# Optimization experiments

Hardware: AMD Instinct MI355X
Metric: run time of the kernel (lower is better)

The kernel has to match this reference:

```python
import jax, jax.numpy as jnp
import numpy as np

N_NODES = 100000
N_EDGES = 1600000
HIDDEN = 128


def setup_inputs() -> dict:
    key = jax.random.key(0)
    ks = jax.random.split(key, 10)
    inp = {
        "hidden_states": jax.random.normal(ks[0], (N_NODES, HIDDEN), dtype=jnp.float32),
        "edges_i": jax.random.randint(ks[1], (2, N_EDGES), 0, N_NODES, dtype=jnp.int64),
        "edges_ii": jax.random.randint(ks[2], (2, N_EDGES), 0, N_NODES, dtype=jnp.int64),
        "edges_iii": jax.random.randint(ks[3], (2, N_EDGES), 0, N_NODES, dtype=jnp.int64),
        "edges_a": jax.random.randint(ks[4], (2, N_EDGES), 0, N_NODES, dtype=jnp.int64),
        # GCNConv weights (hidden -> hidden), no bias, Glorot-like init
        "W_i": jax.random.normal(ks[5], (HIDDEN, HIDDEN), dtype=jnp.float32) / np.sqrt(HIDDEN),
        "W_ii": jax.random.normal(ks[6], (HIDDEN, HIDDEN), dtype=jnp.float32) / np.sqrt(HIDDEN),
        "W_iii": jax.random.normal(ks[7], (HIDDEN, HIDDEN), dtype=jnp.float32) / np.sqrt(HIDDEN),
        "W_a": jax.random.normal(ks[8], (HIDDEN, HIDDEN), dtype=jnp.float32) / np.sqrt(HIDDEN),
    }
    return inp


def _gcn_conv(x, W, edges):
    # GCNConv with normalize=False, add_self_loops=False, bias=False:
    # out[dst] = sum over edges (x @ W)[src]
    xw = x @ W                                   # [N, H] small GEMM
    msg = jnp.take(xw, edges[0], axis=0)         # gather at src: [E, H]
    return jax.ops.segment_sum(msg, edges[1], num_segments=x.shape[0])


def reference(hidden_states, edges_i, edges_ii, edges_iii, edges_a, W_i, W_ii, W_iii, W_a):
    # VariationalNormalEpanechnikovDropout acts as identity in eval mode.
    x = hidden_states
    out = _gcn_conv(x, W_i, edges_i)
    out = out + _gcn_conv(x, W_ii, edges_ii)
    out = out + _gcn_conv(x, W_iii, edges_iii)
    out = out + _gcn_conv(x, W_a, edges_a)
    return out
```

## Files before the change

### kernel.cpp

```cpp
#include <hip/hip_runtime.h>


#define H 128

typedef __bf16 bf16x8 __attribute__((ext_vector_type(8)));
typedef float f32x4 __attribute__((ext_vector_type(4)));

static __device__ __forceinline__ ushort f2bf(float f) {
  union { float f; uint u; } v; v.f = f;
  uint r = (v.u + 0x7FFFu + ((v.u >> 16) & 1u)) >> 16;
  return (ushort)r;
}
static __device__ __forceinline__ float bflo(uint u) {
  union { uint u; float f; } v; v.u = u << 16; return v.f;
}
static __device__ __forceinline__ float bfhi(uint u) {
  union { uint u; float f; } v; v.u = u & 0xFFFF0000u; return v.f;
}

__global__ __launch_bounds__(256) void prep_w(const float* __restrict__ W0,
                                              const float* __restrict__ W1,
                                              const float* __restrict__ W2,
                                              const float* __restrict__ W3,
                                              ushort* __restrict__ Wt) {
  int idx = blockIdx.x * 256 + threadIdx.x;
  int kk = idx & 127;
  int c = (idx >> 7) & 127;
  int k = idx >> 14;
  const float* W = (k == 0) ? W0 : (k == 1) ? W1 : (k == 2) ? W2 : W3;
  Wt[idx] = f2bf(W[kk * 128 + c]);
}

__global__ __launch_bounds__(256) void conv_x(const float4* __restrict__ X4,
                                              uint2* __restrict__ Xb2, int m) {
  int i = blockIdx.x * 256 + threadIdx.x;
  if (i < m) {
    float4 v = X4[i];
    uint2 p;
    p.x = (uint)f2bf(v.x) | ((uint)f2bf(v.y) << 16);
    p.y = (uint)f2bf(v.z) | ((uint)f2bf(v.w) << 16);
    Xb2[i] = p;
  }
}

static __device__ __forceinline__ void fetch_edge(
    int gid, int c1, int c2, int c3,
    const int* d0, const int* d1, const int* d2, const int* d3,
    const int* s0, const int* s1, const int* s2, const int* s3,
    int& dst, int& src, int& k) {
  int i;
  const int *dp, *sp;
  if (gid < c1)      { k = 0; i = gid;      dp = d0; sp = s0; }
  else if (gid < c2) { k = 1; i = gid - c1; dp = d1; sp = s1; }
  else if (gid < c3) { k = 2; i = gid - c2; dp = d2; sp = s2; }
  else               { k = 3; i = gid - c3; dp = d3; sp = s3; }
  dst = dp[i];
  src = sp[i];
}

#define EPB 4096

__global__ __launch_bounds__(256) void part_count(
    const int* __restrict__ d0, const int* __restrict__ d1,
    const int* __restrict__ d2, const int* __restrict__ d3,
    int c1, int c2, int c3, int tot, int nbin, int* __restrict__ hb) {
  __shared__ int lh[512];
  for (int i = threadIdx.x; i < nbin; i += 256) lh[i] = 0;
  __syncthreads();
  int base = blockIdx.x * EPB;
#pragma unroll
  for (int u = 0; u < 16; ++u) {
    int gid = base + u * 256 + threadIdx.x;
    if (gid < tot) {
      int i;
      const int* dp;
      if (gid < c1)      { i = gid;      dp = d0; }
      else if (gid < c2) { i = gid - c1; dp = d1; }
      else if (gid < c3) { i = gid - c2; dp = d2; }
      else               { i = gid - c3; dp = d3; }
      atomicAdd(&lh[dp[i] >> 8], 1);
    }
  }
  __syncthreads();
  int* row = hb + (size_t)blockIdx.x * nbin;
  for (int i = threadIdx.x; i < nbin; i += 256) row[i] = lh[i];
}

__global__ __launch_bounds__(256) void part_scanA(int* __restrict__ hb,
                                                  int nblk, int nbin,
                                                  int* __restrict__ btot) {
  __shared__ int ws4[4];
  const int bin = blockIdx.x;
  const int t = threadIdx.x, lane = t & 63, wid = t >> 6;
  const int C = (nblk + 255) / 256;
  int b0 = t * C;
  int b1 = min(b0 + C, nblk);
  int s = 0;
  for (int b = b0; b < b1; ++b) s += hb[(size_t)b * nbin + bin];
  int incl = s;
#pragma unroll
  for (int d = 1; d < 64; d <<= 1) {
    int x = __shfl_up(incl, d, 64);
    if (lane >= d) incl += x;
  }
  if (lane == 63) ws4[wid] = incl;
  __syncthreads();
  if (t == 0) {
    int run = 0;
#pragma unroll
    for (int i = 0; i < 4; ++i) { int v = ws4[i]; ws4[i] = run; run += v; }
  }
  __syncthreads();
  int run = ws4[wid] + (incl - s);
  for (int b = b0; b < b1; ++b) {
    int v = hb[(size_t)b * nbin + bin];
    hb[(size_t)b * nbin + bin] = run;
    run += v;
  }
  if (t == 255) btot[bin] = run;
}

__global__ __launch_bounds__(512) void part_scanB(const int* __restrict__ btot,
                                                  int* __restrict__ binbase,
                                                  int nbin) {
  __shared__ int ws8[8];
  const int t = threadIdx.x, lane = t & 63, wid = t >> 6;
  int v = (t < nbin) ? btot[t] : 0;
  int incl = v;
#pragma unroll
  for (int d = 1; d < 64; d <<= 1) {
    int x = __shfl_up(incl, d, 64);
    if (lane >= d) incl += x;
  }
  if (lane == 63) ws8[wid] = incl;
  __syncthreads();
  if (t == 0) {
    int run = 0;
#pragma unroll
    for (int i = 0; i < 8; ++i) { int v2 = ws8[i]; ws8[i] = run; run += v2; }
  }
  __syncthreads();
  int excl = ws8[wid] + (incl - v);
  if (t < nbin) binbase[t] = excl;
  if (t == nbin - 1) binbase[nbin] = excl + v;
}

__global__ __launch_bounds__(256) void part_scatter(
    const int* __restrict__ d0, const int* __restrict__ d1,
    const int* __restrict__ d2, const int* __restrict__ d3,
    const int* __restrict__ s0, const int* __restrict__ s1,
    const int* __restrict__ s2, const int* __restrict__ s3,
    int c1, int c2, int c3, int tot, int nbin,
    const int* __restrict__ hb, const int* __restrict__ binbase,
    uint* __restrict__ part) {
  __shared__ int cur[512];
  const int* row = hb + (size_t)blockIdx.x * nbin;
  for (int i = threadIdx.x; i < nbin; i += 256) cur[i] = binbase[i] + row[i];
  __syncthreads();
  int base = blockIdx.x * EPB;
#pragma unroll
  for (int u = 0; u < 16; ++u) {
    int gid = base + u * 256 + threadIdx.x;
    if (gid < tot) {
      int dst, src, k;
      fetch_edge(gid, c1, c2, c3, d0, d1, d2, d3, s0, s1, s2, s3, dst, src, k);
      int pos = atomicAdd(&cur[dst >> 8], 1);
      part[pos] = (uint)src | ((uint)(((dst & 255) << 2) | k) << 17);
    }
  }
}

__global__ __launch_bounds__(1024) void build_bucket(
    const uint* __restrict__ part, const int* __restrict__ binbase,
    int n4, int* __restrict__ rp4, int* __restrict__ col_idx) {
  __shared__ int lh[1024];
  __shared__ int ws16[16];
  const int b = blockIdx.x;
  const int beg = binbase[b], end = binbase[b + 1];
  const int t = threadIdx.x, lane = t & 63, wid = t >> 6;

  lh[t] = 0;
  __syncthreads();
  for (int i = beg + t; i < end; i += 1024)
    atomicAdd(&lh[part[i] >> 17], 1);
  __syncthreads();

  int v = lh[t];
  int incl = v;
#pragma unroll
  for (int d = 1; d < 64; d <<= 1) {
    int x = __shfl_up(incl, d, 64);
    if (lane >= d) incl += x;
  }
  if (lane == 63) ws16[wid] = incl;
  __syncthreads();
  if (t == 0) {
    int run = 0;
#pragma unroll
    for (int i = 0; i < 16; ++i) { int w = ws16[i]; ws16[i] = run; run += w; }
  }
  __syncthreads();
  int excl = ws16[wid] + (incl - v);
  lh[t] = beg + excl;

  int gseg = b * 1024 + t;
  if (gseg <= n4) rp4[gseg] = beg + excl;
  __syncthreads();

  for (int i = beg + t; i < end; i += 1024) {
    uint e = part[i];
    int pos = atomicAdd(&lh[e >> 17], 1);
    col_idx[pos] = (int)(e & 0x1FFFFu);
  }
}

#define ACC8(u)                                                       \
  do {                                                                \
    a0 += bflo((u).x); a1 += bfhi((u).x);                             \
    a2 += bflo((u).y); a3 += bfhi((u).y);                             \
    a4 += bflo((u).z); a5 += bfhi((u).z);                             \
    a6 += bflo((u).w); a7 += bfhi((u).w);                             \
  } while (0)

__global__ __launch_bounds__(256, 8) void gg(const uint* __restrict__ Xb,
                                             const int* __restrict__ rp4,
                                             const int* __restrict__ col_idx,
                                             const ushort* __restrict__ Wt,
                                             float* __restrict__ out, int n) {
  __shared__ uint sS[16][258];

  const int node0 = blockIdx.x * 16;
  const int wave = threadIdx.x >> 6;
  const int lane = threadIdx.x & 63;
  const int g = lane >> 4;
  const int qb = (lane & 15) * 4;

#pragma unroll 1
  for (int i = 0; i < 4; ++i) {
    int local = wave * 4 + i;
    int node = node0 + local;
    if (node < n) {
      const int4 rpv = *(const int4*)(rp4 + (size_t)node * 4);
      const int rpE = rp4[(size_t)node * 4 + 4];
      int pe0 = (rpv.x + lane < rpv.y) ? col_idx[rpv.x + lane] : 0;
      int pe1 = (rpv.y + lane < rpv.z) ? col_idx[rpv.y + lane] : 0;
      int pe2 = (rpv.z + lane < rpv.w) ? col_idx[rpv.z + lane] : 0;
      int pe3 = (rpv.w + lane < rpE)   ? col_idx[rpv.w + lane] : 0;
#pragma unroll
      for (int k = 0; k < 4; ++k) {
        int beg = (k == 0) ? rpv.x : (k == 1) ? rpv.y : (k == 2) ? rpv.z : rpv.w;
        int end = (k == 0) ? rpv.y : (k == 1) ? rpv.z : (k == 2) ? rpv.w : rpE;
        int pe  = (k == 0) ? pe0   : (k == 1) ? pe1   : (k == 2) ? pe2   : pe3;
        int len = end - beg;
        int m = (len > 64) ? 64 : len;
        float a0 = 0.f, a1 = 0.f, a2 = 0.f, a3 = 0.f;
        float a4 = 0.f, a5 = 0.f, a6 = 0.f, a7 = 0.f;
        int s = 0;
        for (; s + 8 <= m; s += 8) {
          int ea = __shfl(pe, s + g, 64);
          int eb = __shfl(pe, s + 4 + g, 64);
          uint4 ua = *(const uint4*)&Xb[(size_t)ea * 64 + qb];
          uint4 ub = *(const uint4*)&Xb[(size_t)eb * 64 + qb];
          ACC8(ua);
          ACC8(ub);
        }
        for (; s < m; s += 4) {
          int li = s + g;
          int e = __shfl(pe, li, 64);
          if (li < m) {
            uint4 u = *(const uint4*)&Xb[(size_t)e * 64 + qb];
            ACC8(u);
          }
        }
        if (len > 64) {
          for (int j = beg + 64; j < end; j += 4) {
            int li = j + g;
            if (li < end) {
              int e = col_idx[li];
              uint4 u = *(const uint4*)&Xb[(size_t)e * 64 + qb];
              ACC8(u);
            }
          }
        }
        a0 += __shfl_xor(a0, 16, 64); a0 += __shfl_xor(a0, 32, 64);
        a1 += __shfl_xor(a1, 16, 64); a1 += __shfl_xor(a1, 32, 64);
        a2 += __shfl_xor(a2, 16, 64); a2 += __shfl_xor(a2, 32, 64);
        a3 += __shfl_xor(a3, 16, 64); a3 += __shfl_xor(a3, 32, 64);
        a4 += __shfl_xor(a4, 16, 64); a4 += __shfl_xor(a4, 32, 64);
        a5 += __shfl_xor(a5, 16, 64); a5 += __shfl_xor(a5, 32, 64);
        a6 += __shfl_xor(a6, 16, 64); a6 += __shfl_xor(a6, 32, 64);
        a7 += __shfl_xor(a7, 16, 64); a7 += __shfl_xor(a7, 32, 64);
        if (lane < 16) {
          uint* drow = &sS[local][k * 64 + qb];
          drow[0] = (uint)f2bf(a0) | ((uint)f2bf(a1) << 16);
          drow[1] = (uint)f2bf(a2) | ((uint)f2bf(a3) << 16);
          drow[2] = (uint)f2bf(a4) | ((uint)f2bf(a5) << 16);
          drow[3] = (uint)f2bf(a6) | ((uint)f2bf(a7) << 16);
        }
      }
    } else {
#pragma unroll
      for (int k = 0; k < 4; ++k) sS[local][k * 64 + lane] = 0u;
    }
  }
  __syncthreads();

  const ushort* sSu = (const ushort*)&sS[0][0];
  const int lr = lane & 15;
  const int lg = lane >> 4;
  const int cf0 = wave * 2;

  f32x4 acc0 = (f32x4)0.f, acc1 = (f32x4)0.f;

#pragma unroll
  for (int kc = 0; kc < 4; ++kc) {
#pragma unroll
    for (int k4 = 0; k4 < 4; ++k4) {
      bf16x8 a = *(const bf16x8*)&sSu[lr * 516 + kc * 128 + k4 * 32 + lg * 8];
      bf16x8 b0 = *(const bf16x8*)&Wt[kc * 16384 + (cf0 * 16 + lr) * 128 + k4 * 32 + lg * 8];
      bf16x8 b1 = *(const bf16x8*)&Wt[kc * 16384 + ((cf0 + 1) * 16 + lr) * 128 + k4 * 32 + lg * 8];
      acc0 = __builtin_amdgcn_mfma_f32_16x16x32_bf16(a, b0, acc0, 0, 0, 0);
      acc1 = __builtin_amdgcn_mfma_f32_16x16x32_bf16(a, b1, acc1, 0, 0, 0);
    }
  }

#pragma unroll
  for (int r = 0; r < 4; ++r) {
    int row = node0 + lg * 4 + r;
    if (row < n) {
      out[(size_t)row * H + cf0 * 16 + lr] = acc0[r];
      out[(size_t)row * H + (cf0 + 1) * 16 + lr] = acc1[r];
    }
  }
}

extern "C" void kernel_launch(void* const* d_in, const int* in_sizes, int n_in,
                              void* d_out, int out_size, void* d_ws, size_t ws_size,
                              hipStream_t stream) {
  const float* X = (const float*)d_in[0];
  const int* edges[4] = {(const int*)d_in[1], (const int*)d_in[2],
                         (const int*)d_in[3], (const int*)d_in[4]};
  const float* Wk[4] = {(const float*)d_in[5], (const float*)d_in[6],
                        (const float*)d_in[7], (const float*)d_in[8]};
  float* out = (float*)d_out;

  int n = in_sizes[0] / H;
  int nE[4];
  int tot = 0;
  for (int k = 0; k < 4; ++k) {
    nE[k] = in_sizes[1 + k] / 2;
    tot += nE[k];
  }
  int c1 = nE[0], c2 = c1 + nE[1], c3 = c2 + nE[2];
  int n4 = n * 4;
  int nbin = (n + 255) / 256;
  int nblk = (tot + EPB - 1) / EPB;

  char* ws = (char*)d_ws;
  size_t off = 0;
  auto take = [&](size_t bytes) -> char* {
    char* p = ws + off;
    off = (off + bytes + 255) & ~(size_t)255;
    return p;
  };
  ushort* Wt = (ushort*)take(4 * 128 * 128 * sizeof(ushort));
  uint* Xb = (uint*)take((size_t)n * H * sizeof(ushort));
  int* hb = (int*)take((size_t)nblk * nbin * sizeof(int));
  int* btot = (int*)take((size_t)nbin * sizeof(int));
  int* binbase = (int*)take((size_t)(nbin + 1) * sizeof(int));
  int* rp4 = (int*)take((size_t)(n4 + 1) * sizeof(int));
  uint* part = (uint*)take((size_t)tot * sizeof(uint));
  int* col_idx = (int*)take((size_t)tot * sizeof(int));

  const int* s0 = edges[0];
  const int* d0 = edges[0] + nE[0];
  const int* s1 = edges[1];
  const int* d1 = edges[1] + nE[1];
  const int* s2 = edges[2];
  const int* d2 = edges[2] + nE[2];
  const int* s3 = edges[3];
  const int* d3 = edges[3] + nE[3];

  prep_w<<<256, 256, 0, stream>>>(Wk[0], Wk[1], Wk[2], Wk[3], Wt);
  conv_x<<<(n * 32 + 255) / 256, 256, 0, stream>>>((const float4*)X, (uint2*)Xb, n * 32);

  part_count<<<nblk, 256, 0, stream>>>(d0, d1, d2, d3, c1, c2, c3, tot, nbin, hb);
  part_scanA<<<nbin, 256, 0, stream>>>(hb, nblk, nbin, btot);
  part_scanB<<<1, 512, 0, stream>>>(btot, binbase, nbin);
  part_scatter<<<nblk, 256, 0, stream>>>(d0, d1, d2, d3, s0, s1, s2, s3,
                                         c1, c2, c3, tot, nbin, hb, binbase, part);
  build_bucket<<<nbin, 1024, 0, stream>>>(part, binbase, n4, rp4, col_idx);

  gg<<<(n + 15) / 16, 256, 0, stream>>>(Xb, rp4, col_idx, Wt, out, n);
}
```

Measured before the change: 416.6 us.

## Merge prep kernels, widen partition bins and edge blocks, unroll gather deeper

Folds the weight-transpose kernel into the X conversion kernel, saving one launch. Bins now cover 512 nodes instead of 256 and each block handles 16384 edges instead of 4096, so the partition stages have fewer histogram rows, fewer blocks and fewer bucket blocks. build_bucket now scans two segments per thread. The gather loop adds a 16-edge unrolled step to keep more loads in flight. The cost is less parallelism in the partition and bucket stages and more register pressure in the gather kernel. rp4 is now written for the padded node range, which the larger workspace allocation covers.

```diff
diff --git a/kernel.cpp b/kernel.cpp
--- a/kernel.cpp
+++ b/kernel.cpp
@@ -2,6 +2,10 @@
 
 
 #define H 128
+#define BSH 9
+#define BNODES (1 << BSH)
+#define SEGB (BNODES * 4)
+#define EPB 16384
 
 typedef __bf16 bf16x8 __attribute__((ext_vector_type(8)));
 typedef float f32x4 __attribute__((ext_vector_type(4)));
@@ -18,21 +22,13 @@
   union { uint u; float f; } v; v.u = u & 0xFFFF0000u; return v.f;
 }
 
-__global__ __launch_bounds__(256) void prep_w(const float* __restrict__ W0,
-                                              const float* __restrict__ W1,
-                                              const float* __restrict__ W2,
-                                              const float* __restrict__ W3,
-                                              ushort* __restrict__ Wt) {
-  int idx = blockIdx.x * 256 + threadIdx.x;
-  int kk = idx & 127;
-  int c = (idx >> 7) & 127;
-  int k = idx >> 14;
-  const float* W = (k == 0) ? W0 : (k == 1) ? W1 : (k == 2) ? W2 : W3;
-  Wt[idx] = f2bf(W[kk * 128 + c]);
-}
-
-__global__ __launch_bounds__(256) void conv_x(const float4* __restrict__ X4,
-                                              uint2* __restrict__ Xb2, int m) {
+__global__ __launch_bounds__(256) void conv_prep(const float4* __restrict__ X4,
+                                                 uint2* __restrict__ Xb2, int m,
+                                                 const float* __restrict__ W0,
+                                                 const float* __restrict__ W1,
+                                                 const float* __restrict__ W2,
+                                                 const float* __restrict__ W3,
+                                                 ushort* __restrict__ Wt) {
   int i = blockIdx.x * 256 + threadIdx.x;
   if (i < m) {
     float4 v = X4[i];
@@ -40,6 +36,13 @@
     p.x = (uint)f2bf(v.x) | ((uint)f2bf(v.y) << 16);
     p.y = (uint)f2bf(v.z) | ((uint)f2bf(v.w) << 16);
     Xb2[i] = p;
+  }
+  if (i < 65536) {
+    int kk = i & 127;
+    int c = (i >> 7) & 127;
+    int k = i >> 14;
+    const float* W = (k == 0) ? W0 : (k == 1) ? W1 : (k == 2) ? W2 : W3;
+    Wt[i] = f2bf(W[kk * 128 + c]);
   }
 }
 
@@ -58,8 +61,6 @@
   src = sp[i];
 }
 
-#define EPB 4096
-
 __global__ __launch_bounds__(256) void part_count(
     const int* __restrict__ d0, const int* __restrict__ d1,
     const int* __restrict__ d2, const int* __restrict__ d3,
@@ -68,8 +69,8 @@
   for (int i = threadIdx.x; i < nbin; i += 256) lh[i] = 0;
   __syncthreads();
   int base = blockIdx.x * EPB;
-#pragma unroll
-  for (int u = 0; u < 16; ++u) {
+#pragma unroll 8
+  for (int u = 0; u < EPB / 256; ++u) {
     int gid = base + u * 256 + threadIdx.x;
     if (gid < tot) {
       int i;
@@ -78,7 +79,7 @@
       else if (gid < c2) { i = gid - c1; dp = d1; }
       else if (gid < c3) { i = gid - c2; dp = d2; }
       else               { i = gid - c3; dp = d3; }
-      atomicAdd(&lh[dp[i] >> 8], 1);
+      atomicAdd(&lh[dp[i] >> BSH], 1);
     }
   }
   __syncthreads();
@@ -158,35 +159,37 @@
   for (int i = threadIdx.x; i < nbin; i += 256) cur[i] = binbase[i] + row[i];
   __syncthreads();
   int base = blockIdx.x * EPB;
-#pragma unroll
-  for (int u = 0; u < 16; ++u) {
+#pragma unroll 8
+  for (int u = 0; u < EPB / 256; ++u) {
     int gid = base + u * 256 + threadIdx.x;
     if (gid < tot) {
       int dst, src, k;
       fetch_edge(gid, c1, c2, c3, d0, d1, d2, d3, s0, s1, s2, s3, dst, src, k);
-      int pos = atomicAdd(&cur[dst >> 8], 1);
-      part[pos] = (uint)src | ((uint)(((dst & 255) << 2) | k) << 17);
+      int pos = atomicAdd(&cur[dst >> BSH], 1);
+      part[pos] = (uint)src | ((uint)(((dst & (BNODES - 1)) << 2) | k) << 17);
     }
   }
 }
 
 __global__ __launch_bounds__(1024) void build_bucket(
     const uint* __restrict__ part, const int* __restrict__ binbase,
-    int n4, int* __restrict__ rp4, int* __restrict__ col_idx) {
-  __shared__ int lh[1024];
+    int* __restrict__ rp4, int* __restrict__ col_idx) {
+  __shared__ int lh[SEGB];
   __shared__ int ws16[16];
   const int b = blockIdx.x;
   const int beg = binbase[b], end = binbase[b + 1];
   const int t = threadIdx.x, lane = t & 63, wid = t >> 6;
 
   lh[t] = 0;
+  lh[t + 1024] = 0;
   __syncthreads();
   for (int i = beg + t; i < end; i += 1024)
     atomicAdd(&lh[part[i] >> 17], 1);
   __syncthreads();
 
-  int v = lh[t];
-  int incl = v;
+  int v0 = lh[2 * t], v1 = lh[2 * t + 1];
+  int s = v0 + v1;
+  int incl = s;
 #pragma unroll
   for (int d = 1; d < 64; d <<= 1) {
     int x = __shfl_up(incl, d, 64);
@@ -200,11 +203,13 @@
     for (int i = 0; i < 16; ++i) { int w = ws16[i]; ws16[i] = run; run += w; }
   }
   __syncthreads();
-  int excl = ws16[wid] + (incl - v);
-  lh[t] = beg + excl;
-
-  int gseg = b * 1024 + t;
-  if (gseg <= n4) rp4[gseg] = beg + excl;
+  int excl = beg + ws16[wid] + (incl - s);
+  lh[2 * t] = excl;
+  lh[2 * t + 1] = excl + v0;
+
+  int gseg = b * SEGB + 2 * t;
+  rp4[gseg] = excl;
+  rp4[gseg + 1] = excl + v0;
   __syncthreads();
 
   for (int i = beg + t; i < end; i += 1024) {
@@ -256,13 +261,23 @@
         float a0 = 0.f, a1 = 0.f, a2 = 0.f, a3 = 0.f;
         float a4 = 0.f, a5 = 0.f, a6 = 0.f, a7 = 0.f;
         int s = 0;
+        for (; s + 16 <= m; s += 16) {
+          int ea = __shfl(pe, s + g, 64);
+          int eb = __shfl(pe, s + 4 + g, 64);
+          int ec = __shfl(pe, s + 8 + g, 64);
+          int ed = __shfl(pe, s + 12 + g, 64);
+          uint4 ua = *(const uint4*)&Xb[(size_t)ea * 64 + qb];
+          uint4 ub = *(const uint4*)&Xb[(size_t)eb * 64 + qb];
+          uint4 uc = *(const uint4*)&Xb[(size_t)ec * 64 + qb];
+          uint4 ud = *(const uint4*)&Xb[(size_t)ed * 64 + qb];
+          ACC8(ua); ACC8(ub); ACC8(uc); ACC8(ud);
+        }
         for (; s + 8 <= m; s += 8) {
           int ea = __shfl(pe, s + g, 64);
           int eb = __shfl(pe, s + 4 + g, 64);
           uint4 ua = *(const uint4*)&Xb[(size_t)ea * 64 + qb];
           uint4 ub = *(const uint4*)&Xb[(size_t)eb * 64 + qb];
-          ACC8(ua);
-          ACC8(ub);
+          ACC8(ua); ACC8(ub);
         }
         for (; s < m; s += 4) {
           int li = s + g;
@@ -352,8 +367,7 @@
     tot += nE[k];
   }
   int c1 = nE[0], c2 = c1 + nE[1], c3 = c2 + nE[2];
-  int n4 = n * 4;
-  int nbin = (n + 255) / 256;
+  int nbin = (n + BNODES - 1) >> BSH;
   int nblk = (tot + EPB - 1) / EPB;
 
   char* ws = (char*)d_ws;
@@ -368,7 +382,7 @@
   int* hb = (int*)take((size_t)nblk * nbin * sizeof(int));
   int* btot = (int*)take((size_t)nbin * sizeof(int));
   int* binbase = (int*)take((size_t)(nbin + 1) * sizeof(int));
-  int* rp4 = (int*)take((size_t)(n4 + 1) * sizeof(int));
+  int* rp4 = (int*)take(((size_t)nbin * SEGB + 1) * sizeof(int));
   uint* part = (uint*)take((size_t)tot * sizeof(uint));
   int* col_idx = (int*)take((size_t)tot * sizeof(int));
 
@@ -381,15 +395,15 @@
   const int* s3 = edges[3];
   const int* d3 = edges[3] + nE[3];
 
-  prep_w<<<256, 256, 0, stream>>>(Wk[0], Wk[1], Wk[2], Wk[3], Wt);
-  conv_x<<<(n * 32 + 255) / 256, 256, 0, stream>>>((const float4*)X, (uint2*)Xb, n * 32);
+  conv_prep<<<(n * 32 + 255) / 256, 256, 0, stream>>>(
+      (const float4*)X, (uint2*)Xb, n * 32, Wk[0], Wk[1], Wk[2], Wk[3], Wt);
 
   part_count<<<nblk, 256, 0, stream>>>(d0, d1, d2, d3, c1, c2, c3, tot, nbin, hb);
   part_scanA<<<nbin, 256, 0, stream>>>(hb, nblk, nbin, btot);
   part_scanB<<<1, 512, 0, stream>>>(btot, binbase, nbin);
   part_scatter<<<nblk, 256, 0, stream>>>(d0, d1, d2, d3, s0, s1, s2, s3,
                                          c1, c2, c3, tot, nbin, hb, binbase, part);
-  build_bucket<<<nbin, 1024, 0, stream>>>(part, binbase, n4, rp4, col_idx);
+  build_bucket<<<nbin, 1024, 0, stream>>>(part, binbase, rp4, col_idx);
 
   gg<<<(n + 15) / 16, 256, 0, stream>>>(Xb, rp4, col_idx, Wt, out, n);
 }
```

Result: no change. 419.0 us (+0.6%).
